# Kernel tuning notes

Hardware: AMD Instinct MI355X
Metric: run time of the kernel (lower is better)

## Reference

```python
import jax, jax.numpy as jnp
import numpy as np


def setup_inputs() -> dict:
    key = jax.random.key(0)
    k1, k2, k3, k4, k5, k6 = jax.random.split(key, 6)
    B, N, C, H = 4096, 64, 192, 6
    NW = 64  # windows per image; must divide B
    TABLE = 225  # (2*8-1)**2
    qkv = jax.random.normal(k1, (B, N, 3 * C), dtype=jnp.float32)
    rpi = jax.random.randint(k2, (N, N), 0, TABLE, dtype=jnp.int64)
    mask = jax.random.normal(k3, (NW, N, N), dtype=jnp.float32)
    rpb_table = jax.random.normal(k4, (TABLE, H), dtype=jnp.float32) * 0.02
    proj_w = jax.random.normal(k5, (C, C), dtype=jnp.float32) * 0.02
    proj_b = jax.random.normal(k6, (C,), dtype=jnp.float32) * 0.02
    return {"qkv": qkv, "rpi": rpi, "mask": mask, "rpb_table": rpb_table,
            "proj_w": proj_w, "proj_b": proj_b}


def reference(qkv, rpi, mask, rpb_table, proj_w, proj_b):
    b_, n, c3 = qkv.shape
    c = c3 // 3
    h = rpb_table.shape[1]           # num_heads
    hd = c // h                      # head_dim
    scale = hd ** (-0.5)
    # (b_, n, 3, h, hd) -> (3, b_, h, n, hd)
    qkv = qkv.reshape(b_, n, 3, h, hd).transpose(2, 0, 3, 1, 4)
    q, k, v = qkv[0] * scale, qkv[1], qkv[2]
    # windowed QK^T: [b_, h, n, n]
    attn = jnp.einsum('bhqd,bhkd->bhqk', q, k)
    # relative position bias gather: rpi [n,n] -> [h,n,n]
    bias = rpb_table[rpi].transpose(2, 0, 1)
    attn = attn + bias[None]
    # shift-window mask add
    nw = mask.shape[0]
    attn = attn.reshape(b_ // nw, nw, h, n, n) + mask[None, :, None]
    attn = attn.reshape(b_, h, n, n)
    attn = jax.nn.softmax(attn, axis=-1)
    # AV then output projection
    out = jnp.einsum('bhqk,bhkd->bhqd', attn, v)
    out = out.transpose(0, 2, 1, 3).reshape(b_, n, c)
    return out @ proj_w.T + proj_b
```

## Files before the change

kernel.cpp:

```cpp
#include <hip/hip_runtime.h>
#include <stdint.h>

typedef __bf16 bf16x8 __attribute__((ext_vector_type(8)));
typedef float f32x4 __attribute__((ext_vector_type(4)));

__device__ __forceinline__ unsigned short f2bf(float f) {
    union { float f; uint32_t u; } v; v.f = f;
    uint32_t u = v.u;
    return (unsigned short)((u + 0x7FFFu + ((u >> 16) & 1u)) >> 16);
}

#define QS_STRIDE 40
#define VT_STRIDE 72
#define PS_STRIDE 72
#define XS_STRIDE 200

__global__ void prep_all(const int* __restrict__ rpi32,
                         const float* __restrict__ mask,
                         const float* __restrict__ rpb,
                         const float* __restrict__ proj_w,
                         float* __restrict__ bm,
                         unsigned short* __restrict__ wf) {
    int bid = blockIdx.x;
    int tid = threadIdx.x;
    if (bid < 6144) {
        __shared__ int is64_s;
        if (tid == 0) {
            int s = 0;
            #pragma unroll
            for (int i = 0; i < 16; ++i) s |= rpi32[2 * i + 1];
            is64_s = (s == 0);
        }
        __syncthreads();
        int g = bid * 256 + tid;
        int wh = g >> 12;
        int e  = g & 4095;
        int c = e >> 6, r = e & 63;
        int h = wh % 6, w = wh / 6;
        int rc = r * 64 + c;
        int rv = is64_s ? rpi32[2 * rc] : rpi32[rc];
        bm[g] = mask[w * 4096 + rc] + rpb[rv * 6 + h];
    } else {
        int g = (bid - 6144) * 256 + tid;
        int e = g & 7;
        int lane = (g >> 3) & 63;
        int kkct = g >> 9;
        int kk = kkct / 12, ct = kkct % 12;
        int co = ct * 16 + (lane & 15);
        int ki = kk * 32 + (lane >> 4) * 8 + e;
        wf[g] = f2bf(proj_w[co * 192 + ki]);
    }
}


__global__ __launch_bounds__(256, 3)
void winattn_fast(const float* __restrict__ qkv,
                  const float* __restrict__ bm,
                  const unsigned short* __restrict__ wf,
                  const float* __restrict__ proj_b,
                  float* __restrict__ out) {
    __shared__ __align__(16) unsigned short x_s[64 * XS_STRIDE];
    __shared__ __align__(16) unsigned short u_s[7424];
    __shared__ __align__(16) unsigned short p_s[4 * 16 * PS_STRIDE];

    unsigned short* q_s  = u_s;
    unsigned short* k_s  = u_s + 2560;
    unsigned short* vT_s = u_s + 5120;

    const int tid  = threadIdx.x;
    const int b    = blockIdx.x;
    const int lane = tid & 63;
    const int wv   = tid >> 6;
    const int l16  = lane & 15;
    const int lhi  = lane >> 4;
    const int qbase = wv * 16;
    const float scale = 0.17677669529663687f;

    const float* qkv_b = qkv + (size_t)b * 64 * 576;
    const float* bm_w  = bm + (size_t)(b & 63) * 6 * 4096;

    const int tokA = tid >> 3;
    const int dA   = (tid & 7) << 2;
    const float4* gA = (const float4*)(qkv_b + tokA * 576 + dA);
    const float4* gB = (const float4*)(qkv_b + (tokA + 32) * 576 + dA);

    float4 q0, k0, v0, q1, k1, v1;

#define LOADH(h_)  do { int o = (h_) * 8;                         \
        q0 = gA[o];      k0 = gA[o + 48]; v0 = gA[o + 96];        \
        q1 = gB[o];      k1 = gB[o + 48]; v1 = gB[o + 96]; } while (0)

#define STOREH() do {                                             \
        ushort4 qh, kh;                                           \
        qh.x = f2bf(q0.x * scale); qh.y = f2bf(q0.y * scale);     \
        qh.z = f2bf(q0.z * scale); qh.w = f2bf(q0.w * scale);     \
        kh.x = f2bf(k0.x); kh.y = f2bf(k0.y);                     \
        kh.z = f2bf(k0.z); kh.w = f2bf(k0.w);                     \
        *(ushort4*)&q_s[tokA * QS_STRIDE + dA] = qh;              \
        *(ushort4*)&k_s[tokA * QS_STRIDE + dA] = kh;              \
        vT_s[(dA + 0) * VT_STRIDE + tokA] = f2bf(v0.x);           \
        vT_s[(dA + 1) * VT_STRIDE + tokA] = f2bf(v0.y);           \
        vT_s[(dA + 2) * VT_STRIDE + tokA] = f2bf(v0.z);           \
        vT_s[(dA + 3) * VT_STRIDE + tokA] = f2bf(v0.w);           \
        qh.x = f2bf(q1.x * scale); qh.y = f2bf(q1.y * scale);     \
        qh.z = f2bf(q1.z * scale); qh.w = f2bf(q1.w * scale);     \
        kh.x = f2bf(k1.x); kh.y = f2bf(k1.y);                     \
        kh.z = f2bf(k1.z); kh.w = f2bf(k1.w);                     \
        *(ushort4*)&q_s[(tokA + 32) * QS_STRIDE + dA] = qh;       \
        *(ushort4*)&k_s[(tokA + 32) * QS_STRIDE + dA] = kh;       \
        vT_s[(dA + 0) * VT_STRIDE + tokA + 32] = f2bf(v1.x);      \
        vT_s[(dA + 1) * VT_STRIDE + tokA + 32] = f2bf(v1.y);      \
        vT_s[(dA + 2) * VT_STRIDE + tokA + 32] = f2bf(v1.z);      \
        vT_s[(dA + 3) * VT_STRIDE + tokA + 32] = f2bf(v1.w); } while (0)

    LOADH(0);
    STOREH();

    unsigned short* pw = p_s + wv * 16 * PS_STRIDE;

    for (int h = 0; h < 6; ++h) {
        __syncthreads();
        if (h < 5) LOADH(h + 1);

        const float* bmh = bm_w + h * 4096;
        float4 bv[4];
        #pragma unroll
        for (int nt = 0; nt < 4; ++nt)
            bv[nt] = *(const float4*)&bmh[(nt * 16 + l16) * 64 + qbase + lhi * 4];

        bf16x8 aq = *(const bf16x8*)&q_s[(qbase + l16) * QS_STRIDE + lhi * 8];
        float lg[4][4];
        #pragma unroll
        for (int nt = 0; nt < 4; ++nt) {
            bf16x8 bk = *(const bf16x8*)&k_s[(nt * 16 + l16) * QS_STRIDE + lhi * 8];
            f32x4 c = {0.f, 0.f, 0.f, 0.f};
            c = __builtin_amdgcn_mfma_f32_16x16x32_bf16(aq, bk, c, 0, 0, 0);
            lg[nt][0] = c[0] + bv[nt].x; lg[nt][1] = c[1] + bv[nt].y;
            lg[nt][2] = c[2] + bv[nt].z; lg[nt][3] = c[3] + bv[nt].w;
        }

        float srow[4];
        float p[4][4];
        #pragma unroll
        for (int j = 0; j < 4; ++j) {
            float m = fmaxf(fmaxf(lg[0][j], lg[1][j]), fmaxf(lg[2][j], lg[3][j]));
            #pragma unroll
            for (int o = 1; o < 16; o <<= 1) m = fmaxf(m, __shfl_xor(m, o, 64));
            float s = 0.f;
            #pragma unroll
            for (int nt = 0; nt < 4; ++nt) { p[nt][j] = __expf(lg[nt][j] - m); s += p[nt][j]; }
            #pragma unroll
            for (int o = 1; o < 16; o <<= 1) s += __shfl_xor(s, o, 64);
            srow[j] = s;
        }

        #pragma unroll
        for (int nt = 0; nt < 4; ++nt)
            #pragma unroll
            for (int j = 0; j < 4; ++j)
                pw[(lhi * 4 + j) * PS_STRIDE + nt * 16 + l16] = f2bf(p[nt][j]);

        f32x4 xo[2] = {{0.f,0.f,0.f,0.f},{0.f,0.f,0.f,0.f}};
        #pragma unroll
        for (int kk = 0; kk < 2; ++kk) {
            bf16x8 pa = *(const bf16x8*)&pw[l16 * PS_STRIDE + kk * 32 + lhi * 8];
            #pragma unroll
            for (int dt = 0; dt < 2; ++dt) {
                bf16x8 vb = *(const bf16x8*)&vT_s[(dt * 16 + l16) * VT_STRIDE + kk * 32 + lhi * 8];
                xo[dt] = __builtin_amdgcn_mfma_f32_16x16x32_bf16(pa, vb, xo[dt], 0, 0, 0);
            }
        }
        #pragma unroll
        for (int j = 0; j < 4; ++j) {
            float inv = __builtin_amdgcn_rcpf(srow[j]);
            int n = qbase + lhi * 4 + j;
            #pragma unroll
            for (int dt = 0; dt < 2; ++dt)
                x_s[n * XS_STRIDE + h * 32 + dt * 16 + l16] = f2bf(xo[dt][j] * inv);
        }

        __syncthreads();
        if (h < 5) STOREH();
    }
#undef LOADH
#undef STOREH

    f32x4 oacc[12];
    #pragma unroll
    for (int ct = 0; ct < 12; ++ct) oacc[ct] = (f32x4){0.f, 0.f, 0.f, 0.f};
    #pragma unroll
    for (int kk = 0; kk < 6; ++kk) {
        bf16x8 ax = *(const bf16x8*)&x_s[(qbase + l16) * XS_STRIDE + kk * 32 + lhi * 8];
        #pragma unroll
        for (int ct = 0; ct < 12; ++ct) {
            bf16x8 bw = *(const bf16x8*)&wf[((kk * 12 + ct) * 64 + lane) * 8];
            oacc[ct] = __builtin_amdgcn_mfma_f32_16x16x32_bf16(ax, bw, oacc[ct], 0, 0, 0);
        }
    }
    float* outb = out + (size_t)b * 64 * 192;
    #pragma unroll
    for (int ct = 0; ct < 12; ++ct) {
        int co = ct * 16 + l16;
        float bias = proj_b[co];
        #pragma unroll
        for (int j = 0; j < 4; ++j) {
            int n = qbase + lhi * 4 + j;
            outb[n * 192 + co] = oacc[ct][j] + bias;
        }
    }
}


#define WS_STRIDE 40

__global__ __launch_bounds__(256)
void winattn_fused(const float* __restrict__ qkv,
                   const int* __restrict__ rpi32,
                   const float* __restrict__ mask,
                   const float* __restrict__ rpb_table,
                   const float* __restrict__ proj_w,
                   const float* __restrict__ proj_b,
                   float* __restrict__ out) {
    __shared__ __align__(16) unsigned short x_s[64 * XS_STRIDE];
    __shared__ __align__(16) unsigned short u_s[12032];
    __shared__ float rpb_s[225];
    __shared__ int rpi_is64_s;

    unsigned short* q_s  = u_s;
    unsigned short* k_s  = u_s + 2560;
    unsigned short* vT_s = u_s + 5120;
    unsigned short* p_s  = u_s + 7424;
    unsigned short* w_s  = u_s;

    const int tid  = threadIdx.x;
    const int b    = blockIdx.x;
    const int lane = tid & 63;
    const int wv   = tid >> 6;
    const int l16  = lane & 15;
    const int lhi  = lane >> 4;
    const int qbase = wv * 16;
    const float scale = 0.17677669529663687f;

    if (tid == 0) {
        int s = 0;
        #pragma unroll
        for (int i = 0; i < 16; ++i) s |= rpi32[2 * i + 1];
        rpi_is64_s = (s == 0) ? 1 : 0;
    }

    const float* maskw = mask + (size_t)(b & 63) * 4096;
    const float* qkv_b = qkv + (size_t)b * 64 * 576;

    for (int h = 0; h < 6; ++h) {
        for (int idx = tid; idx < 64 * 8; idx += 256) {
            int tok = idx >> 3, d = (idx & 7) << 2;
            const float4* base = (const float4*)(qkv_b + tok * 576 + h * 32 + d);
            float4 qv = base[0];
            float4 kv = base[48];
            float4 vv = base[96];
            ushort4 qh, kh;
            qh.x = f2bf(qv.x * scale); qh.y = f2bf(qv.y * scale);
            qh.z = f2bf(qv.z * scale); qh.w = f2bf(qv.w * scale);
            kh.x = f2bf(kv.x); kh.y = f2bf(kv.y); kh.z = f2bf(kv.z); kh.w = f2bf(kv.w);
            *(ushort4*)&q_s[tok * QS_STRIDE + d] = qh;
            *(ushort4*)&k_s[tok * QS_STRIDE + d] = kh;
            vT_s[(d + 0) * VT_STRIDE + tok] = f2bf(vv.x);
            vT_s[(d + 1) * VT_STRIDE + tok] = f2bf(vv.y);
            vT_s[(d + 2) * VT_STRIDE + tok] = f2bf(vv.z);
            vT_s[(d + 3) * VT_STRIDE + tok] = f2bf(vv.w);
        }
        if (tid < 225) rpb_s[tid] = rpb_table[tid * 6 + h];
        __syncthreads();
        const int is64 = rpi_is64_s;

        bf16x8 aq = *(const bf16x8*)&q_s[(qbase + l16) * QS_STRIDE + lhi * 8];
        float lg[4][4];
        #pragma unroll
        for (int nt = 0; nt < 4; ++nt) {
            bf16x8 bk = *(const bf16x8*)&k_s[(nt * 16 + l16) * QS_STRIDE + lhi * 8];
            f32x4 c = {0.f, 0.f, 0.f, 0.f};
            c = __builtin_amdgcn_mfma_f32_16x16x32_bf16(aq, bk, c, 0, 0, 0);
            #pragma unroll
            for (int j = 0; j < 4; ++j) lg[nt][j] = c[j];
        }
        #pragma unroll
        for (int nt = 0; nt < 4; ++nt) {
            int c = nt * 16 + l16;
            #pragma unroll
            for (int j = 0; j < 4; ++j) {
                int r = qbase + lhi * 4 + j;
                int e = r * 64 + c;
                int rv = is64 ? rpi32[2 * e] : rpi32[e];
                lg[nt][j] += rpb_s[rv] + maskw[e];
            }
        }
        float srow[4];
        float p[4][4];
        #pragma unroll
        for (int j = 0; j < 4; ++j) {
            float m = fmaxf(fmaxf(lg[0][j], lg[1][j]), fmaxf(lg[2][j], lg[3][j]));
            #pragma unroll
            for (int o = 1; o < 16; o <<= 1) m = fmaxf(m, __shfl_xor(m, o, 64));
            float s = 0.f;
            #pragma unroll
            for (int nt = 0; nt < 4; ++nt) { p[nt][j] = __expf(lg[nt][j] - m); s += p[nt][j]; }
            #pragma unroll
            for (int o = 1; o < 16; o <<= 1) s += __shfl_xor(s, o, 64);
            srow[j] = s;
        }
        __syncthreads();
        unsigned short* pw = p_s + wv * 16 * PS_STRIDE;
        #pragma unroll
        for (int nt = 0; nt < 4; ++nt)
            #pragma unroll
            for (int j = 0; j < 4; ++j)
                pw[(lhi * 4 + j) * PS_STRIDE + nt * 16 + l16] = f2bf(p[nt][j]);
        __syncthreads();

        f32x4 xo[2] = {{0.f,0.f,0.f,0.f},{0.f,0.f,0.f,0.f}};
        #pragma unroll
        for (int kk = 0; kk < 2; ++kk) {
            bf16x8 pa = *(const bf16x8*)&pw[l16 * PS_STRIDE + kk * 32 + lhi * 8];
            #pragma unroll
            for (int dt = 0; dt < 2; ++dt) {
                bf16x8 vb = *(const bf16x8*)&vT_s[(dt * 16 + l16) * VT_STRIDE + kk * 32 + lhi * 8];
                xo[dt] = __builtin_amdgcn_mfma_f32_16x16x32_bf16(pa, vb, xo[dt], 0, 0, 0);
            }
        }
        #pragma unroll
        for (int j = 0; j < 4; ++j) {
            float inv = 1.f / srow[j];
            int n = qbase + lhi * 4 + j;
            #pragma unroll
            for (int dt = 0; dt < 2; ++dt)
                x_s[n * XS_STRIDE + h * 32 + dt * 16 + l16] = f2bf(xo[dt][j] * inv);
        }
        __syncthreads();
    }

    f32x4 oacc[12];
    #pragma unroll
    for (int ct = 0; ct < 12; ++ct) oacc[ct] = (f32x4){0.f, 0.f, 0.f, 0.f};
    for (int kk = 0; kk < 6; ++kk) {
        for (int idx = tid; idx < 192 * 8; idx += 256) {
            int co = idx >> 3, d = (idx & 7) << 2;
            float4 wvv = *(const float4*)(proj_w + co * 192 + kk * 32 + d);
            ushort4 wh;
            wh.x = f2bf(wvv.x); wh.y = f2bf(wvv.y); wh.z = f2bf(wvv.z); wh.w = f2bf(wvv.w);
            *(ushort4*)&w_s[co * WS_STRIDE + d] = wh;
        }
        __syncthreads();
        bf16x8 ax = *(const bf16x8*)&x_s[(qbase + l16) * XS_STRIDE + kk * 32 + lhi * 8];
        #pragma unroll
        for (int ct = 0; ct < 12; ++ct) {
            bf16x8 bw = *(const bf16x8*)&w_s[(ct * 16 + l16) * WS_STRIDE + lhi * 8];
            oacc[ct] = __builtin_amdgcn_mfma_f32_16x16x32_bf16(ax, bw, oacc[ct], 0, 0, 0);
        }
        __syncthreads();
    }
    float* outb = out + (size_t)b * 64 * 192;
    #pragma unroll
    for (int ct = 0; ct < 12; ++ct) {
        int co = ct * 16 + l16;
        float bias = proj_b[co];
        #pragma unroll
        for (int j = 0; j < 4; ++j) {
            int n = qbase + lhi * 4 + j;
            outb[n * 192 + co] = oacc[ct][j] + bias;
        }
    }
}

extern "C" void kernel_launch(void* const* d_in, const int* in_sizes, int n_in,
                              void* d_out, int out_size, void* d_ws, size_t ws_size,
                              hipStream_t stream) {
    (void)in_sizes; (void)n_in; (void)out_size;
    const float* qkv       = (const float*)d_in[0];
    const int*   rpi       = (const int*)d_in[1];
    const float* mask      = (const float*)d_in[2];
    const float* rpb_table = (const float*)d_in[3];
    const float* proj_w    = (const float*)d_in[4];
    const float* proj_b    = (const float*)d_in[5];
    float* out = (float*)d_out;

    const size_t BM_BYTES = (size_t)64 * 6 * 4096 * sizeof(float);
    const size_t WF_BYTES = (size_t)36864 * sizeof(unsigned short);

    if (ws_size >= BM_BYTES + WF_BYTES) {
        float* bmp = (float*)d_ws;
        unsigned short* wfp = (unsigned short*)((char*)d_ws + BM_BYTES);
        prep_all<<<6144 + 144, 256, 0, stream>>>(rpi, mask, rpb_table, proj_w, bmp, wfp);
        winattn_fast<<<4096, 256, 0, stream>>>(qkv, bmp, wfp, proj_b, out);
    } else {
        winattn_fused<<<4096, 256, 0, stream>>>(qkv, rpi, mask, rpb_table, proj_w, proj_b, out);
    }
}
```

Baseline: 213.0 us.

## Fuse per-head output projection and load Q/K directly into MFMA registers

The winattn_fast kernel now reads Q and K straight from global memory into registers and converts them to bf16 MFMA operands, so they no longer pass through shared memory. Only V is staged, through a double-buffered transposed LDS buffer that needs a single barrier per head. The output projection is accumulated per head from a small per-wave xh buffer instead of from a full 64x192 x_s tile. With less LDS in use, launch bounds go from 3 to 4 blocks per CU, at the cost of redundant global K loads across waves and 48 accumulator registers held live through the head loop.

After: 335.2 us. +57.4%, slower.

```diff
diff --git a/kernel.cpp b/kernel.cpp
--- a/kernel.cpp
+++ b/kernel.cpp
@@ -10,10 +10,18 @@
     return (unsigned short)((u + 0x7FFFu + ((u >> 16) & 1u)) >> 16);
 }
 
-#define QS_STRIDE 40
+__device__ __forceinline__ bf16x8 cvt8(float4 a, float4 b, float s) {
+    union { unsigned short u[8]; bf16x8 v; } r;
+    r.u[0] = f2bf(a.x * s); r.u[1] = f2bf(a.y * s);
+    r.u[2] = f2bf(a.z * s); r.u[3] = f2bf(a.w * s);
+    r.u[4] = f2bf(b.x * s); r.u[5] = f2bf(b.y * s);
+    r.u[6] = f2bf(b.z * s); r.u[7] = f2bf(b.w * s);
+    return r.v;
+}
+
 #define VT_STRIDE 72
 #define PS_STRIDE 72
-#define XS_STRIDE 200
+#define XH_STRIDE 40
 
 __global__ void prep_all(const int* __restrict__ rpi32,
                          const float* __restrict__ mask,
@@ -53,19 +61,15 @@
 }
 
 
-__global__ __launch_bounds__(256, 3)
+__global__ __launch_bounds__(256, 4)
 void winattn_fast(const float* __restrict__ qkv,
                   const float* __restrict__ bm,
                   const unsigned short* __restrict__ wf,
                   const float* __restrict__ proj_b,
                   float* __restrict__ out) {
-    __shared__ __align__(16) unsigned short x_s[64 * XS_STRIDE];
-    __shared__ __align__(16) unsigned short u_s[7424];
+    __shared__ __align__(16) unsigned short vT_s[2][32 * VT_STRIDE];
     __shared__ __align__(16) unsigned short p_s[4 * 16 * PS_STRIDE];
-
-    unsigned short* q_s  = u_s;
-    unsigned short* k_s  = u_s + 2560;
-    unsigned short* vT_s = u_s + 5120;
+    __shared__ __align__(16) unsigned short xh_s[4 * 16 * XH_STRIDE];
 
     const int tid  = threadIdx.x;
     const int b    = blockIdx.x;
@@ -81,58 +85,60 @@
 
     const int tokA = tid >> 3;
     const int dA   = (tid & 7) << 2;
-    const float4* gA = (const float4*)(qkv_b + tokA * 576 + dA);
-    const float4* gB = (const float4*)(qkv_b + (tokA + 32) * 576 + dA);
-
-    float4 q0, k0, v0, q1, k1, v1;
-
-#define LOADH(h_)  do { int o = (h_) * 8;                         \
-        q0 = gA[o];      k0 = gA[o + 48]; v0 = gA[o + 96];        \
-        q1 = gB[o];      k1 = gB[o + 48]; v1 = gB[o + 96]; } while (0)
-
-#define STOREH() do {                                             \
-        ushort4 qh, kh;                                           \
-        qh.x = f2bf(q0.x * scale); qh.y = f2bf(q0.y * scale);     \
-        qh.z = f2bf(q0.z * scale); qh.w = f2bf(q0.w * scale);     \
-        kh.x = f2bf(k0.x); kh.y = f2bf(k0.y);                     \
-        kh.z = f2bf(k0.z); kh.w = f2bf(k0.w);                     \
-        *(ushort4*)&q_s[tokA * QS_STRIDE + dA] = qh;              \
-        *(ushort4*)&k_s[tokA * QS_STRIDE + dA] = kh;              \
-        vT_s[(dA + 0) * VT_STRIDE + tokA] = f2bf(v0.x);           \
-        vT_s[(dA + 1) * VT_STRIDE + tokA] = f2bf(v0.y);           \
-        vT_s[(dA + 2) * VT_STRIDE + tokA] = f2bf(v0.z);           \
-        vT_s[(dA + 3) * VT_STRIDE + tokA] = f2bf(v0.w);           \
-        qh.x = f2bf(q1.x * scale); qh.y = f2bf(q1.y * scale);     \
-        qh.z = f2bf(q1.z * scale); qh.w = f2bf(q1.w * scale);     \
-        kh.x = f2bf(k1.x); kh.y = f2bf(k1.y);                     \
-        kh.z = f2bf(k1.z); kh.w = f2bf(k1.w);                     \
-        *(ushort4*)&q_s[(tokA + 32) * QS_STRIDE + dA] = qh;       \
-        *(ushort4*)&k_s[(tokA + 32) * QS_STRIDE + dA] = kh;       \
-        vT_s[(dA + 0) * VT_STRIDE + tokA + 32] = f2bf(v1.x);      \
-        vT_s[(dA + 1) * VT_STRIDE + tokA + 32] = f2bf(v1.y);      \
-        vT_s[(dA + 2) * VT_STRIDE + tokA + 32] = f2bf(v1.z);      \
-        vT_s[(dA + 3) * VT_STRIDE + tokA + 32] = f2bf(v1.w); } while (0)
-
-    LOADH(0);
-    STOREH();
+    const float4* vA = (const float4*)(qkv_b + tokA * 576 + dA + 384);
+    const float4* vB = (const float4*)(qkv_b + (tokA + 32) * 576 + dA + 384);
+
+    float4 v0, v1;
+
+#define LOADV(h_) do { v0 = vA[(h_) * 8]; v1 = vB[(h_) * 8]; } while (0)
+#define STOREV(buf) do {                                    \
+        (buf)[(dA + 0) * VT_STRIDE + tokA] = f2bf(v0.x);    \
+        (buf)[(dA + 1) * VT_STRIDE + tokA] = f2bf(v0.y);    \
+        (buf)[(dA + 2) * VT_STRIDE + tokA] = f2bf(v0.z);    \
+        (buf)[(dA + 3) * VT_STRIDE + tokA] = f2bf(v0.w);    \
+        (buf)[(dA + 0) * VT_STRIDE + tokA + 32] = f2bf(v1.x); \
+        (buf)[(dA + 1) * VT_STRIDE + tokA + 32] = f2bf(v1.y); \
+        (buf)[(dA + 2) * VT_STRIDE + tokA + 32] = f2bf(v1.z); \
+        (buf)[(dA + 3) * VT_STRIDE + tokA + 32] = f2bf(v1.w); } while (0)
+
+    LOADV(0);
+    STOREV(vT_s[0]);
+    LOADV(1);
 
     unsigned short* pw = p_s + wv * 16 * PS_STRIDE;
+    unsigned short* xh = xh_s + wv * 16 * XH_STRIDE;
+
+    f32x4 oacc[12];
+    #pragma unroll
+    for (int ct = 0; ct < 12; ++ct) oacc[ct] = (f32x4){0.f, 0.f, 0.f, 0.f};
 
     for (int h = 0; h < 6; ++h) {
         __syncthreads();
-        if (h < 5) LOADH(h + 1);
-
+        if (h < 5) STOREV(vT_s[(h + 1) & 1]);
+        if (h < 4) LOADV(h + 2);
+
+        const float* qptr = qkv_b + (qbase + l16) * 576 + h * 32 + lhi * 8;
+        float4 qf0 = ((const float4*)qptr)[0];
+        float4 qf1 = ((const float4*)qptr)[1];
+        float4 kf[8];
+        #pragma unroll
+        for (int nt = 0; nt < 4; ++nt) {
+            const float* kptr = qkv_b + 192 + (nt * 16 + l16) * 576 + h * 32 + lhi * 8;
+            kf[2 * nt]     = ((const float4*)kptr)[0];
+            kf[2 * nt + 1] = ((const float4*)kptr)[1];
+        }
         const float* bmh = bm_w + h * 4096;
         float4 bv[4];
         #pragma unroll
         for (int nt = 0; nt < 4; ++nt)
             bv[nt] = *(const float4*)&bmh[(nt * 16 + l16) * 64 + qbase + lhi * 4];
 
-        bf16x8 aq = *(const bf16x8*)&q_s[(qbase + l16) * QS_STRIDE + lhi * 8];
+        bf16x8 aq = cvt8(qf0, qf1, scale);
+
         float lg[4][4];
         #pragma unroll
         for (int nt = 0; nt < 4; ++nt) {
-            bf16x8 bk = *(const bf16x8*)&k_s[(nt * 16 + l16) * QS_STRIDE + lhi * 8];
+            bf16x8 bk = cvt8(kf[2 * nt], kf[2 * nt + 1], 1.0f);
             f32x4 c = {0.f, 0.f, 0.f, 0.f};
             c = __builtin_amdgcn_mfma_f32_16x16x32_bf16(aq, bk, c, 0, 0, 0);
             lg[nt][0] = c[0] + bv[nt].x; lg[nt][1] = c[1] + bv[nt].y;
@@ -140,7 +146,6 @@
         }
 
         float srow[4];
-        float p[4][4];
         #pragma unroll
         for (int j = 0; j < 4; ++j) {
             float m = fmaxf(fmaxf(lg[0][j], lg[1][j]), fmaxf(lg[2][j], lg[3][j]));
@@ -148,7 +153,7 @@
             for (int o = 1; o < 16; o <<= 1) m = fmaxf(m, __shfl_xor(m, o, 64));
             float s = 0.f;
             #pragma unroll
-            for (int nt = 0; nt < 4; ++nt) { p[nt][j] = __expf(lg[nt][j] - m); s += p[nt][j]; }
+            for (int nt = 0; nt < 4; ++nt) { lg[nt][j] = __expf(lg[nt][j] - m); s += lg[nt][j]; }
             #pragma unroll
             for (int o = 1; o < 16; o <<= 1) s += __shfl_xor(s, o, 64);
             srow[j] = s;
@@ -158,45 +163,37 @@
         for (int nt = 0; nt < 4; ++nt)
             #pragma unroll
             for (int j = 0; j < 4; ++j)
-                pw[(lhi * 4 + j) * PS_STRIDE + nt * 16 + l16] = f2bf(p[nt][j]);
-
+                pw[(lhi * 4 + j) * PS_STRIDE + nt * 16 + l16] = f2bf(lg[nt][j]);
+
+        const unsigned short* vt = vT_s[h & 1];
         f32x4 xo[2] = {{0.f,0.f,0.f,0.f},{0.f,0.f,0.f,0.f}};
         #pragma unroll
         for (int kk = 0; kk < 2; ++kk) {
             bf16x8 pa = *(const bf16x8*)&pw[l16 * PS_STRIDE + kk * 32 + lhi * 8];
             #pragma unroll
             for (int dt = 0; dt < 2; ++dt) {
-                bf16x8 vb = *(const bf16x8*)&vT_s[(dt * 16 + l16) * VT_STRIDE + kk * 32 + lhi * 8];
+                bf16x8 vb = *(const bf16x8*)&vt[(dt * 16 + l16) * VT_STRIDE + kk * 32 + lhi * 8];
                 xo[dt] = __builtin_amdgcn_mfma_f32_16x16x32_bf16(pa, vb, xo[dt], 0, 0, 0);
             }
         }
         #pragma unroll
         for (int j = 0; j < 4; ++j) {
             float inv = __builtin_amdgcn_rcpf(srow[j]);
-            int n = qbase + lhi * 4 + j;
             #pragma unroll
             for (int dt = 0; dt < 2; ++dt)
-                x_s[n * XS_STRIDE + h * 32 + dt * 16 + l16] = f2bf(xo[dt][j] * inv);
-        }
-
-        __syncthreads();
-        if (h < 5) STOREH();
-    }
-#undef LOADH
-#undef STOREH
-
-    f32x4 oacc[12];
-    #pragma unroll
-    for (int ct = 0; ct < 12; ++ct) oacc[ct] = (f32x4){0.f, 0.f, 0.f, 0.f};
-    #pragma unroll
-    for (int kk = 0; kk < 6; ++kk) {
-        bf16x8 ax = *(const bf16x8*)&x_s[(qbase + l16) * XS_STRIDE + kk * 32 + lhi * 8];
+                xh[(lhi * 4 + j) * XH_STRIDE + dt * 16 + l16] = f2bf(xo[dt][j] * inv);
+        }
+
+        bf16x8 ax = *(const bf16x8*)&xh[l16 * XH_STRIDE + lhi * 8];
         #pragma unroll
         for (int ct = 0; ct < 12; ++ct) {
-            bf16x8 bw = *(const bf16x8*)&wf[((kk * 12 + ct) * 64 + lane) * 8];
+            bf16x8 bw = *(const bf16x8*)&wf[((h * 12 + ct) * 64 + lane) * 8];
             oacc[ct] = __builtin_amdgcn_mfma_f32_16x16x32_bf16(ax, bw, oacc[ct], 0, 0, 0);
         }
     }
+#undef LOADV
+#undef STOREV
+
     float* outb = out + (size_t)b * 64 * 192;
     #pragma unroll
     for (int ct = 0; ct < 12; ++ct) {
@@ -211,6 +208,8 @@
 }
 
 
+#define QS_STRIDE 40
+#define XS_STRIDE 200
 #define WS_STRIDE 40
 
 __global__ __launch_bounds__(256)
```
